# Kernel optimization log

Hardware: AMD Instinct MI355X
Metric: run time of the kernel (lower is better)

Reference implementation:

```python
import jax, jax.numpy as jnp
import numpy as np

NEG_SLOPE = 0.2


def setup_inputs() -> dict:
    key = jax.random.key(0)
    ks = jax.random.split(key, 12)
    N, D = 50000, 256
    H, C = 4, 128          # heads, per-head channels; H*C = gnn_hidden_dim = 512
    E = 800000
    edge_index = jax.random.randint(ks[0], (2, E), 0, N, dtype=jnp.int64)
    edge_weight = jax.random.uniform(ks[1], (E,), dtype=jnp.float32)
    s = 1.0 / np.sqrt(D)
    return {
        'edge_index': edge_index,
        'edge_weight': edge_weight,
        'emb':     jax.random.normal(ks[2], (N, D), jnp.float32),
        'W':       jax.random.normal(ks[3], (D, H * C), jnp.float32) * s,
        'att_src': jax.random.normal(ks[4], (H, C), jnp.float32) * s,
        'att_dst': jax.random.normal(ks[5], (H, C), jnp.float32) * s,
        'att_edge': jax.random.normal(ks[6], (H, C), jnp.float32) * s,
        'W_edge':  jax.random.normal(ks[7], (1, H * C), jnp.float32),
        'bias':    jnp.zeros((H * C,), jnp.float32),
        'W_out':   jax.random.normal(ks[8], (H * C, D), jnp.float32) * s,
        'b_out':   jnp.zeros((D,), jnp.float32),
    }


def reference(edge_index, edge_weight, emb, W, att_src, att_dst, att_edge,
              W_edge, bias, W_out, b_out):
    N, D = emb.shape
    H, C = att_src.shape
    src, dst = edge_index[0], edge_index[1]
    E = src.shape[0]

    # GATConv: shared linear projection for src and dst (in_channels is int)
    x = (emb @ W).reshape(N, H, C)                     # [N,H,C]

    # add self loops; edge_attr for loops = per-dst mean of incoming edge_attr
    ones = jnp.ones((E,), emb.dtype)
    cnt = jax.ops.segment_sum(ones, dst, num_segments=N)
    ea_mean = jax.ops.segment_sum(edge_weight, dst, num_segments=N) / jnp.maximum(cnt, 1.0)
    loop = jnp.arange(N, dtype=src.dtype)
    src_f = jnp.concatenate([src, loop])
    dst_f = jnp.concatenate([dst, loop])
    ea = jnp.concatenate([edge_weight, ea_mean])[:, None]   # [E+N, 1]

    e_feat = (ea @ W_edge).reshape(-1, H, C)            # [E+N,H,C]

    a_src = jnp.einsum('nhc,hc->nh', x, att_src)        # [N,H]
    a_dst = jnp.einsum('nhc,hc->nh', x, att_dst)
    a_e = jnp.einsum('ehc,hc->eh', e_feat, att_edge)    # [E+N,H]

    alpha = jax.nn.leaky_relu(a_src[src_f] + a_dst[dst_f] + a_e, NEG_SLOPE)
    # segment softmax over destination neighborhoods
    m = jax.ops.segment_max(alpha, dst_f, num_segments=N)
    alpha = jnp.exp(alpha - m[dst_f])
    denom = jax.ops.segment_sum(alpha, dst_f, num_segments=N)
    alpha = alpha / (denom[dst_f] + 1e-16)              # [E+N,H]

    msg = x[src_f] * alpha[..., None]                   # [E+N,H,C]
    out = jax.ops.segment_sum(msg, dst_f, num_segments=N).reshape(N, H * C) + bias

    return out @ W_out + b_out                          # [N,D]
```

## Files before the change

### kernel.cpp

```cpp
#include <hip/hip_runtime.h>
#include <cstdint>
#include <cstddef>

#define NEG_SLOPE 0.2f
#define HC 512
#define NH 4
#define CAP 64

typedef __attribute__((ext_vector_type(8))) short bf16x8;
typedef __attribute__((ext_vector_type(4))) float f32x4;

__device__ inline float lrelu(float z) { return z > 0.f ? z : NEG_SLOPE * z; }

__device__ inline unsigned short f2bf(float f) {
    unsigned u = __float_as_uint(f);
    u += 0x7FFFu + ((u >> 16) & 1u);
    return (unsigned short)(u >> 16);
}
__device__ inline float bflo(unsigned v) { return __uint_as_float(v << 16); }
__device__ inline float bfhi(unsigned v) { return __uint_as_float(v & 0xffff0000u); }

#define GLOAD16(gp, lp) \
    __builtin_amdgcn_global_load_lds( \
        (const __attribute__((address_space(1))) unsigned int*)(const void*)(gp), \
        (__attribute__((address_space(3))) unsigned int*)(void*)(lp), 16, 0, 0)

__global__ __launch_bounds__(256) void wprep_kernel(
        const float* __restrict__ W, const float* __restrict__ W_out,
        const float* __restrict__ att_s, const float* __restrict__ att_d,
        const float* __restrict__ W_edge, const float* __restrict__ att_edge,
        const float* __restrict__ bias, const float* __restrict__ b_out,
        const int* __restrict__ ei, const float* __restrict__ ew, int E,
        unsigned short* __restrict__ Wb, unsigned short* __restrict__ WoT,
        float* __restrict__ watt, float* __restrict__ bc4, float* __restrict__ sh,
        int* __restrict__ cnt, int2* __restrict__ csr2) {
    int b = blockIdx.x, t = threadIdx.x;
    if (b < 128) {
        int i = b * 256 + t;
        float4 v = reinterpret_cast<const float4*>(W)[i];
        ushort4 o;
        o.x = f2bf(v.x); o.y = f2bf(v.y); o.z = f2bf(v.z); o.w = f2bf(v.w);
        reinterpret_cast<ushort4*>(Wb)[i] = o;
    } else if (b < 640) {
        int idx = (b - 128) * 256 + t;
        int r = idx >> 8, c = idx & 255;
        WoT[(size_t)c * 512 + r] = f2bf(W_out[idx]);
    } else if (b < 648) {
        int i = b - 640;
        int h = i & 3;
        const float* att = (i < 4) ? att_s : att_d;
        float s = 0.f;
        for (int c = 0; c < 128; ++c)
            s += W[(size_t)t * HC + h * 128 + c] * att[h * 128 + c];
        watt[i * 256 + t] = s;
    } else if (b < 652) {
        int part = b - 648;
        int j0 = part * 128;
        float s = (part == 0) ? b_out[t] : 0.f;
        for (int j = j0; j < j0 + 128; ++j)
            s += bias[j] * W_out[(size_t)j * 256 + t];
        bc4[part * 256 + t] = s;
    } else if (b == 652) {
        if (t < NH) {
            float s = 0.f;
            for (int c = 0; c < 128; ++c)
                s += W_edge[t * 128 + c] * att_edge[t * 128 + c];
            sh[t] = s;
        }
    } else {
        int lane = t & 63;
        unsigned long long nzm = __ballot(ei[2 * lane + 1] != 0);
        int is64 = (nzm == 0ull) ? 1 : 0;
        int base = (b - 653) * 1024;

        int dv[4], sv[4];
        float wv[4];
        bool ok[4];
        #pragma unroll
        for (int r = 0; r < 4; ++r) {
            int e = base + r * 256 + t;
            ok[r] = (e < E);
            if (ok[r]) {
                size_t de = (size_t)E + e;
                dv[r] = is64 ? ei[2 * de] : ei[de];
                sv[r] = is64 ? ei[2 * (size_t)e] : ei[e];
                wv[r] = ew[e];
            }
        }
        int pos[4];
        #pragma unroll
        for (int r = 0; r < 4; ++r)
            if (ok[r]) pos[r] = atomicAdd(&cnt[dv[r]], 1);
        #pragma unroll
        for (int r = 0; r < 4; ++r)
            if (ok[r] && pos[r] < CAP)
                csr2[(size_t)dv[r] * CAP + pos[r]] =
                    make_int2(sv[r], __float_as_int(wv[r]));
    }
}

__global__ __launch_bounds__(256) void mt_kernel(
        const unsigned short* __restrict__ WoT, const unsigned short* __restrict__ Wb,
        unsigned short* __restrict__ MT) {
    __shared__ __align__(16) unsigned short As[128 * 64];
    __shared__ __align__(16) unsigned short Bs[128 * 64];
    int b = blockIdx.x, t = threadIdx.x;
    int lane = t & 63, w = t >> 6;
    int bn = (b & 1) * 128, bm = ((b >> 1) & 1) * 128, z = b >> 2;
    const unsigned short* A  = WoT + (size_t)z * 128;
    const unsigned short* BT = Wb  + (size_t)z * 128;
    int wr = w >> 1, wc = w & 1;

    f32x4 acc[4][4];
    #pragma unroll
    for (int i = 0; i < 4; ++i)
        #pragma unroll
        for (int j = 0; j < 4; ++j)
            acc[i][j] = (f32x4){0.f, 0.f, 0.f, 0.f};

    int lr = lane & 15, kb = lane >> 4;
    int q = lane & 7;

    for (int k0 = 0; k0 < 128; k0 += 64) {
        #pragma unroll
        for (int p = 0; p < 4; ++p) {
            int row = p * 32 + w * 8 + (lane >> 3);
            int ce  = ((q ^ (row & 7)) << 3) + k0;
            int ob  = p * 4096 + w * 1024;
            GLOAD16(A  + (size_t)(bm + row) * 512 + ce, (char*)As + ob);
            GLOAD16(BT + (size_t)(bn + row) * 512 + ce, (char*)Bs + ob);
        }
        __syncthreads();
        #pragma unroll
        for (int kk = 0; kk < 2; ++kk) {
            bf16x8 a[4], bfr[4];
            #pragma unroll
            for (int i = 0; i < 4; ++i) {
                int row = wr * 64 + i * 16 + lr;
                a[i] = *reinterpret_cast<const bf16x8*>(
                    &As[row * 64 + (((kk * 4 + kb) ^ (row & 7)) << 3)]);
            }
            #pragma unroll
            for (int j = 0; j < 4; ++j) {
                int row = wc * 64 + j * 16 + lr;
                bfr[j] = *reinterpret_cast<const bf16x8*>(
                    &Bs[row * 64 + (((kk * 4 + kb) ^ (row & 7)) << 3)]);
            }
            #pragma unroll
            for (int i = 0; i < 4; ++i)
                #pragma unroll
                for (int j = 0; j < 4; ++j)
                    acc[i][j] = __builtin_amdgcn_mfma_f32_16x16x32_bf16(a[i], bfr[j], acc[i][j], 0, 0, 0);
        }
        __syncthreads();
    }
    int rg = lane >> 4;
    #pragma unroll
    for (int i = 0; i < 4; ++i)
        #pragma unroll
        for (int r = 0; r < 4; ++r) {
            int row = bm + wr * 64 + i * 16 + rg * 4 + r;
            #pragma unroll
            for (int j = 0; j < 4; ++j) {
                int col = bn + wc * 64 + j * 16 + lr;
                MT[(size_t)row * 1024 + z * 256 + col] = f2bf(acc[i][j][r]);
            }
        }
}

__global__ __launch_bounds__(256) void embcast_kernel(
        const float4* __restrict__ embf4, const float* __restrict__ watt,
        uint2* __restrict__ embq, float* __restrict__ a_src,
        float* __restrict__ a_dst, int N) {
    int t = threadIdx.x;
    int wid = t >> 6, lane = t & 63;
    #pragma unroll
    for (int j = 0; j < 4; ++j) {
        int n = blockIdx.x * 16 + wid * 4 + j;
        if (n >= N) break;
        float4 v = embf4[(size_t)n * 64 + lane];
        uint2 o;
        o.x = (unsigned)f2bf(v.x) | ((unsigned)f2bf(v.y) << 16);
        o.y = (unsigned)f2bf(v.z) | ((unsigned)f2bf(v.w) << 16);
        embq[(size_t)n * 64 + lane] = o;
        float r[8];
        #pragma unroll
        for (int i = 0; i < 8; ++i) {
            float4 wv = reinterpret_cast<const float4*>(watt)[i * 64 + lane];
            r[i] = v.x * wv.x + v.y * wv.y + v.z * wv.z + v.w * wv.w;
        }
        #pragma unroll
        for (int off = 32; off > 0; off >>= 1) {
            #pragma unroll
            for (int i = 0; i < 8; ++i) r[i] += __shfl_xor(r[i], off);
        }
        if (lane == 0) {
            size_t bofs = (size_t)n * 4;
            a_src[bofs + 0] = r[0]; a_src[bofs + 1] = r[1];
            a_src[bofs + 2] = r[2]; a_src[bofs + 3] = r[3];
            a_dst[bofs + 0] = r[4]; a_dst[bofs + 1] = r[5];
            a_dst[bofs + 2] = r[6]; a_dst[bofs + 3] = r[7];
        }
    }
}

#define EFMA(W_, V_) { \
    float e0_ = bflo(V_.x), e1_ = bfhi(V_.x), e2_ = bflo(V_.y), e3_ = bfhi(V_.y); \
    a00 += W_.x * e0_; a01 += W_.x * e1_; a02 += W_.x * e2_; a03 += W_.x * e3_; \
    a10 += W_.y * e0_; a11 += W_.y * e1_; a12 += W_.y * e2_; a13 += W_.y * e3_; \
    a20 += W_.z * e0_; a21 += W_.z * e1_; a22 += W_.z * e2_; a23 += W_.z * e3_; \
    a30 += W_.w * e0_; a31 += W_.w * e1_; a32 += W_.w * e2_; a33 += W_.w * e3_; \
    den0 += W_.x; den1 += W_.y; den2 += W_.z; den3 += W_.w; }

__global__ __launch_bounds__(256) void agg_kernel(
        const uint2* __restrict__ embq, const float* __restrict__ a_src,
        const float* __restrict__ a_dst, const int* __restrict__ cnt,
        const float* __restrict__ sh, const int2* __restrict__ csr2,
        uint2* __restrict__ aggn, int N) {
    int wid = threadIdx.x >> 6, lane = threadIdx.x & 63;
    int n = blockIdx.x * 4 + wid;
    if (n >= N) return;
    int deg = cnt[n];
    int m = deg < CAP ? deg : CAP;

    __shared__ int s_src[4][64];
    __shared__ __align__(16) float s_alpha[4][64][4];

    int2 p;
    float wgt = 0.f;
    if (lane < m) {
        p = csr2[(size_t)n * CAP + lane];
        wgt = __int_as_float(p.y);
    }
    float wsl = wgt;
    #pragma unroll
    for (int o = 32; o > 0; o >>= 1) wsl += __shfl_xor(wsl, o);
    float eam = wsl / fmaxf((float)deg, 1.f);

    float ad0 = a_dst[(size_t)n * 4 + 0], ad1 = a_dst[(size_t)n * 4 + 1];
    float ad2 = a_dst[(size_t)n * 4 + 2], ad3 = a_dst[(size_t)n * 4 + 3];
    float sh0 = sh[0], sh1 = sh[1], sh2 = sh[2], sh3 = sh[3];
    float es0 = __expf(lrelu(a_src[(size_t)n * 4 + 0] + ad0 + eam * sh0));
    float es1 = __expf(lrelu(a_src[(size_t)n * 4 + 1] + ad1 + eam * sh1));
    float es2 = __expf(lrelu(a_src[(size_t)n * 4 + 2] + ad2 + eam * sh2));
    float es3 = __expf(lrelu(a_src[(size_t)n * 4 + 3] + ad3 + eam * sh3));

    uint2 xv = embq[(size_t)n * 64 + lane];
    float d0 = bflo(xv.x), d1 = bfhi(xv.x), d2 = bflo(xv.y), d3 = bfhi(xv.y);

    float a00 = es0 * d0, a01 = es0 * d1, a02 = es0 * d2, a03 = es0 * d3;
    float a10 = es1 * d0, a11 = es1 * d1, a12 = es1 * d2, a13 = es1 * d3;
    float a20 = es2 * d0, a21 = es2 * d1, a22 = es2 * d2, a23 = es2 * d3;
    float a30 = es3 * d0, a31 = es3 * d1, a32 = es3 * d2, a33 = es3 * d3;
    float den0 = es0, den1 = es1, den2 = es2, den3 = es3;

    if (lane < m) {
        int s = p.x;
        s_src[wid][lane] = s;
        float4 as4 = *reinterpret_cast<const float4*>(&a_src[(size_t)s * 4]);
        s_alpha[wid][lane][0] = __expf(lrelu(as4.x + ad0 + wgt * sh0));
        s_alpha[wid][lane][1] = __expf(lrelu(as4.y + ad1 + wgt * sh1));
        s_alpha[wid][lane][2] = __expf(lrelu(as4.z + ad2 + wgt * sh2));
        s_alpha[wid][lane][3] = __expf(lrelu(as4.w + ad3 + wgt * sh3));
    }
    int e2 = 0;
    for (; e2 + 2 <= m; e2 += 2) {
        int s0 = s_src[wid][e2], s1 = s_src[wid][e2 + 1];
        float4 w0 = *reinterpret_cast<const float4*>(s_alpha[wid][e2]);
        float4 w1 = *reinterpret_cast<const float4*>(s_alpha[wid][e2 + 1]);
        uint2 v0 = embq[(size_t)s0 * 64 + lane];
        uint2 v1 = embq[(size_t)s1 * 64 + lane];
        EFMA(w0, v0); EFMA(w1, v1);
    }
    if (e2 < m) {
        int s0 = s_src[wid][e2];
        float4 w0 = *reinterpret_cast<const float4*>(s_alpha[wid][e2]);
        uint2 v0 = embq[(size_t)s0 * 64 + lane];
        EFMA(w0, v0);
    }

    float i0 = 1.f / (den0 + 1e-16f), i1 = 1.f / (den1 + 1e-16f);
    float i2 = 1.f / (den2 + 1e-16f), i3 = 1.f / (den3 + 1e-16f);
    size_t base = (size_t)n * 256 + lane;
    uint2 o;
    o.x = (unsigned)f2bf(a00 * i0) | ((unsigned)f2bf(a01 * i0) << 16);
    o.y = (unsigned)f2bf(a02 * i0) | ((unsigned)f2bf(a03 * i0) << 16);
    aggn[base] = o;
    o.x = (unsigned)f2bf(a10 * i1) | ((unsigned)f2bf(a11 * i1) << 16);
    o.y = (unsigned)f2bf(a12 * i1) | ((unsigned)f2bf(a13 * i1) << 16);
    aggn[base + 64] = o;
    o.x = (unsigned)f2bf(a20 * i2) | ((unsigned)f2bf(a21 * i2) << 16);
    o.y = (unsigned)f2bf(a22 * i2) | ((unsigned)f2bf(a23 * i2) << 16);
    aggn[base + 128] = o;
    o.x = (unsigned)f2bf(a30 * i3) | ((unsigned)f2bf(a31 * i3) << 16);
    o.y = (unsigned)f2bf(a32 * i3) | ((unsigned)f2bf(a33 * i3) << 16);
    aggn[base + 192] = o;
}

__global__ __launch_bounds__(512) void gemm_out_kernel(
        const unsigned short* __restrict__ A,
        const unsigned short* __restrict__ BT,
        const float* __restrict__ bc4, float* __restrict__ C, int M) {
    __shared__ __align__(16) unsigned short As[128 * 64];
    __shared__ __align__(16) unsigned short Bs[256 * 64];
    int tid = threadIdx.x;
    int lane = tid & 63, w = tid >> 6;
    int bm = blockIdx.x * 128;
    int wr = w >> 2, wc = w & 3;

    f32x4 acc[4][4];
    #pragma unroll
    for (int i = 0; i < 4; ++i)
        #pragma unroll
        for (int j = 0; j < 4; ++j)
            acc[i][j] = (f32x4){0.f, 0.f, 0.f, 0.f};

    int lr = lane & 15, kb = lane >> 4;
    int q = lane & 7;

    for (int k0 = 0; k0 < 1024; k0 += 64) {
        #pragma unroll
        for (int p = 0; p < 2; ++p) {
            int row = p * 64 + w * 8 + (lane >> 3);
            int ce  = ((q ^ (row & 7)) << 3) + k0;
            int ob  = p * 8192 + w * 1024;
            int gr = bm + row; if (gr >= M) gr = M - 1;
            GLOAD16(A + (size_t)gr * 1024 + ce, (char*)As + ob);
        }
        #pragma unroll
        for (int p = 0; p < 4; ++p) {
            int row = p * 64 + w * 8 + (lane >> 3);
            int ce  = ((q ^ (row & 7)) << 3) + k0;
            int ob  = p * 8192 + w * 1024;
            GLOAD16(BT + (size_t)row * 1024 + ce, (char*)Bs + ob);
        }
        __syncthreads();

        #pragma unroll
        for (int kk = 0; kk < 2; ++kk) {
            bf16x8 a[4], b[4];
            #pragma unroll
            for (int i = 0; i < 4; ++i) {
                int row = wr * 64 + i * 16 + lr;
                a[i] = *reinterpret_cast<const bf16x8*>(
                    &As[row * 64 + (((kk * 4 + kb) ^ (row & 7)) << 3)]);
            }
            #pragma unroll
            for (int j = 0; j < 4; ++j) {
                int row = wc * 64 + j * 16 + lr;
                b[j] = *reinterpret_cast<const bf16x8*>(
                    &Bs[row * 64 + (((kk * 4 + kb) ^ (row & 7)) << 3)]);
            }
            #pragma unroll
            for (int i = 0; i < 4; ++i)
                #pragma unroll
                for (int j = 0; j < 4; ++j)
                    acc[i][j] = __builtin_amdgcn_mfma_f32_16x16x32_bf16(a[i], b[j], acc[i][j], 0, 0, 0);
        }
        __syncthreads();
    }

    int rg = lane >> 4;
    #pragma unroll
    for (int i = 0; i < 4; ++i) {
        #pragma unroll
        for (int r = 0; r < 4; ++r) {
            int row = bm + wr * 64 + i * 16 + rg * 4 + r;
            if (row >= M) continue;
            #pragma unroll
            for (int j = 0; j < 4; ++j) {
                int col = wc * 64 + j * 16 + lr;
                float bval = bc4[col] + bc4[256 + col] + bc4[512 + col] + bc4[768 + col];
                C[(size_t)row * 256 + col] = acc[i][j][r] + bval;
            }
        }
    }
}

extern "C" void kernel_launch(void* const* d_in, const int* in_sizes, int n_in,
                              void* d_out, int out_size, void* d_ws, size_t ws_size,
                              hipStream_t stream) {
    const int*   edge_index  = (const int*)d_in[0];
    const float* edge_weight = (const float*)d_in[1];
    const float* emb         = (const float*)d_in[2];
    const float* W           = (const float*)d_in[3];
    const float* att_src     = (const float*)d_in[4];
    const float* att_dst     = (const float*)d_in[5];
    const float* att_edge    = (const float*)d_in[6];
    const float* W_edge      = (const float*)d_in[7];
    const float* bias        = (const float*)d_in[8];
    const float* W_out       = (const float*)d_in[9];
    const float* b_out       = (const float*)d_in[10];
    float* out = (float*)d_out;

    const int E = in_sizes[1];
    const int D = 256;
    const int N = in_sizes[2] / D;
    const int mb = (N + 127) / 128;
    const int nEmb = (N + 15) / 16;
    const int nEdge4 = (E + 1023) / 1024;

    char* ws = (char*)d_ws;
    size_t off = 0;
    auto alloc = [&](size_t bytes) {
        size_t o = off;
        off += (bytes + 255) & ~(size_t)255;
        return o;
    };
    unsigned short* embb  = (unsigned short*)(ws + alloc((size_t)N * D * 2));
    unsigned short* aggn  = (unsigned short*)(ws + alloc((size_t)N * 1024 * 2));
    unsigned short* Wb    = (unsigned short*)(ws + alloc((size_t)D * HC * 2));
    unsigned short* WoT   = (unsigned short*)(ws + alloc((size_t)HC * D * 2));
    unsigned short* MT    = (unsigned short*)(ws + alloc((size_t)256 * 1024 * 2));
    float* watt    = (float*)(ws + alloc(2048 * 4));
    float* bc4     = (float*)(ws + alloc(1024 * 4));
    float* a_src   = (float*)(ws + alloc((size_t)N * 4 * 4));
    float* a_dst   = (float*)(ws + alloc((size_t)N * 4 * 4));
    float* sh      = (float*)(ws + alloc(64));
    size_t zbytes  = (size_t)N * 4;
    size_t zoff    = alloc(zbytes);
    int*   cnt     = (int*)(ws + zoff);
    int2*  csr2    = (int2*)(ws + alloc((size_t)N * CAP * 8));
    (void)ws_size; (void)n_in; (void)out_size;

    hipMemsetAsync(ws + zoff, 0, zbytes, stream);

    wprep_kernel<<<653 + nEdge4, 256, 0, stream>>>(
        W, W_out, att_src, att_dst, W_edge, att_edge, bias, b_out,
        edge_index, edge_weight, E, Wb, WoT, watt, bc4, sh, cnt, csr2);

    mt_kernel<<<16, 256, 0, stream>>>(WoT, Wb, MT);

    embcast_kernel<<<nEmb, 256, 0, stream>>>(
        (const float4*)emb, watt, (uint2*)embb, a_src, a_dst, N);

    agg_kernel<<<(N + 3) / 4, 256, 0, stream>>>(
        (const uint2*)embb, a_src, a_dst, cnt, sh, csr2, (uint2*)aggn, N);

    gemm_out_kernel<<<mb, 512, 0, stream>>>(aggn, MT, bc4, out, N);
}
```

Measured before the change: 226.5 us.

## Merge CSR build, weight-product GEMM and emb cast into one launch; fold memset into prep

The count-array memset moves into the weight-prep kernel as extra zeroing blocks. The edge CSR build, the small MT GEMM and the embedding bf16 cast/attention-dot kernel become one multi-role kernel dispatched by block index. This removes two launches and a memset and lets independent stages overlap on the GPU. The cost is that every block of the fused kernel reserves 32KB of shared memory, which may lower occupancy for the edge and cast blocks.

```diff
diff --git a/kernel.cpp b/kernel.cpp
--- a/kernel.cpp
+++ b/kernel.cpp
@@ -25,15 +25,14 @@
         (const __attribute__((address_space(1))) unsigned int*)(const void*)(gp), \
         (__attribute__((address_space(3))) unsigned int*)(void*)(lp), 16, 0, 0)
 
-__global__ __launch_bounds__(256) void wprep_kernel(
+__global__ __launch_bounds__(256) void prep0_kernel(
         const float* __restrict__ W, const float* __restrict__ W_out,
         const float* __restrict__ att_s, const float* __restrict__ att_d,
         const float* __restrict__ W_edge, const float* __restrict__ att_edge,
         const float* __restrict__ bias, const float* __restrict__ b_out,
-        const int* __restrict__ ei, const float* __restrict__ ew, int E,
         unsigned short* __restrict__ Wb, unsigned short* __restrict__ WoT,
         float* __restrict__ watt, float* __restrict__ bc4, float* __restrict__ sh,
-        int* __restrict__ cnt, int2* __restrict__ csr2) {
+        uint4* __restrict__ zptr, int zcount) {
     int b = blockIdx.x, t = threadIdx.x;
     if (b < 128) {
         int i = b * 256 + t;
@@ -68,10 +67,27 @@
             sh[t] = s;
         }
     } else {
+        int idx = (b - 653) * 256 + t;
+        if (idx < zcount) zptr[idx] = (uint4){0u, 0u, 0u, 0u};
+    }
+}
+
+__global__ __launch_bounds__(256) void mega_kernel(
+        const int* __restrict__ ei, const float* __restrict__ ew, int E,
+        int* __restrict__ cnt, int2* __restrict__ csr2,
+        const unsigned short* __restrict__ WoT, const unsigned short* __restrict__ Wb,
+        unsigned short* __restrict__ MT,
+        const float4* __restrict__ embf4, const float* __restrict__ watt,
+        uint2* __restrict__ embq, float* __restrict__ a_src,
+        float* __restrict__ a_dst, int N, int nEdge4) {
+    __shared__ __align__(16) char smem[32768];
+    int b = blockIdx.x, t = threadIdx.x;
+
+    if (b < nEdge4) {
         int lane = t & 63;
         unsigned long long nzm = __ballot(ei[2 * lane + 1] != 0);
         int is64 = (nzm == 0ull) ? 1 : 0;
-        int base = (b - 653) * 1024;
+        int base = b * 1024;
 
         int dv[4], sv[4];
         float wv[4];
@@ -96,110 +112,101 @@
             if (ok[r] && pos[r] < CAP)
                 csr2[(size_t)dv[r] * CAP + pos[r]] =
                     make_int2(sv[r], __float_as_int(wv[r]));
-    }
-}
-
-__global__ __launch_bounds__(256) void mt_kernel(
-        const unsigned short* __restrict__ WoT, const unsigned short* __restrict__ Wb,
-        unsigned short* __restrict__ MT) {
-    __shared__ __align__(16) unsigned short As[128 * 64];
-    __shared__ __align__(16) unsigned short Bs[128 * 64];
-    int b = blockIdx.x, t = threadIdx.x;
-    int lane = t & 63, w = t >> 6;
-    int bn = (b & 1) * 128, bm = ((b >> 1) & 1) * 128, z = b >> 2;
-    const unsigned short* A  = WoT + (size_t)z * 128;
-    const unsigned short* BT = Wb  + (size_t)z * 128;
-    int wr = w >> 1, wc = w & 1;
-
-    f32x4 acc[4][4];
-    #pragma unroll
-    for (int i = 0; i < 4; ++i)
-        #pragma unroll
-        for (int j = 0; j < 4; ++j)
-            acc[i][j] = (f32x4){0.f, 0.f, 0.f, 0.f};
-
-    int lr = lane & 15, kb = lane >> 4;
-    int q = lane & 7;
-
-    for (int k0 = 0; k0 < 128; k0 += 64) {
-        #pragma unroll
-        for (int p = 0; p < 4; ++p) {
-            int row = p * 32 + w * 8 + (lane >> 3);
-            int ce  = ((q ^ (row & 7)) << 3) + k0;
-            int ob  = p * 4096 + w * 1024;
-            GLOAD16(A  + (size_t)(bm + row) * 512 + ce, (char*)As + ob);
-            GLOAD16(BT + (size_t)(bn + row) * 512 + ce, (char*)Bs + ob);
-        }
-        __syncthreads();
-        #pragma unroll
-        for (int kk = 0; kk < 2; ++kk) {
-            bf16x8 a[4], bfr[4];
-            #pragma unroll
-            for (int i = 0; i < 4; ++i) {
-                int row = wr * 64 + i * 16 + lr;
-                a[i] = *reinterpret_cast<const bf16x8*>(
-                    &As[row * 64 + (((kk * 4 + kb) ^ (row & 7)) << 3)]);
-            }
-            #pragma unroll
-            for (int j = 0; j < 4; ++j) {
-                int row = wc * 64 + j * 16 + lr;
-                bfr[j] = *reinterpret_cast<const bf16x8*>(
-                    &Bs[row * 64 + (((kk * 4 + kb) ^ (row & 7)) << 3)]);
-            }
-            #pragma unroll
-            for (int i = 0; i < 4; ++i)
-                #pragma unroll
-                for (int j = 0; j < 4; ++j)
-                    acc[i][j] = __builtin_amdgcn_mfma_f32_16x16x32_bf16(a[i], bfr[j], acc[i][j], 0, 0, 0);
-        }
-        __syncthreads();
-    }
-    int rg = lane >> 4;
-    #pragma unroll
-    for (int i = 0; i < 4; ++i)
-        #pragma unroll
-        for (int r = 0; r < 4; ++r) {
-            int row = bm + wr * 64 + i * 16 + rg * 4 + r;
-            #pragma unroll
-            for (int j = 0; j < 4; ++j) {
-                int col = bn + wc * 64 + j * 16 + lr;
-                MT[(size_t)row * 1024 + z * 256 + col] = f2bf(acc[i][j][r]);
-            }
-        }
-}
-
-__global__ __launch_bounds__(256) void embcast_kernel(
-        const float4* __restrict__ embf4, const float* __restrict__ watt,
-        uint2* __restrict__ embq, float* __restrict__ a_src,
-        float* __restrict__ a_dst, int N) {
-    int t = threadIdx.x;
-    int wid = t >> 6, lane = t & 63;
-    #pragma unroll
-    for (int j = 0; j < 4; ++j) {
-        int n = blockIdx.x * 16 + wid * 4 + j;
-        if (n >= N) break;
-        float4 v = embf4[(size_t)n * 64 + lane];
-        uint2 o;
-        o.x = (unsigned)f2bf(v.x) | ((unsigned)f2bf(v.y) << 16);
-        o.y = (unsigned)f2bf(v.z) | ((unsigned)f2bf(v.w) << 16);
-        embq[(size_t)n * 64 + lane] = o;
-        float r[8];
-        #pragma unroll
-        for (int i = 0; i < 8; ++i) {
-            float4 wv = reinterpret_cast<const float4*>(watt)[i * 64 + lane];
-            r[i] = v.x * wv.x + v.y * wv.y + v.z * wv.z + v.w * wv.w;
-        }
-        #pragma unroll
-        for (int off = 32; off > 0; off >>= 1) {
-            #pragma unroll
-            for (int i = 0; i < 8; ++i) r[i] += __shfl_xor(r[i], off);
-        }
-        if (lane == 0) {
-            size_t bofs = (size_t)n * 4;
-            a_src[bofs + 0] = r[0]; a_src[bofs + 1] = r[1];
-            a_src[bofs + 2] = r[2]; a_src[bofs + 3] = r[3];
-            a_dst[bofs + 0] = r[4]; a_dst[bofs + 1] = r[5];
-            a_dst[bofs + 2] = r[6]; a_dst[bofs + 3] = r[7];
+    } else if (b < nEdge4 + 16) {
+        int bb = b - nEdge4;
+        unsigned short* As = (unsigned short*)smem;
+        unsigned short* Bs = (unsigned short*)(smem + 16384);
+        int lane = t & 63, w = t >> 6;
+        int bn = (bb & 1) * 128, bm = ((bb >> 1) & 1) * 128, z = bb >> 2;
+        const unsigned short* A  = WoT + (size_t)z * 128;
+        const unsigned short* BT = Wb  + (size_t)z * 128;
+        int wr = w >> 1, wc = w & 1;
+
+        f32x4 acc[4][4];
+        #pragma unroll
+        for (int i = 0; i < 4; ++i)
+            #pragma unroll
+            for (int j = 0; j < 4; ++j)
+                acc[i][j] = (f32x4){0.f, 0.f, 0.f, 0.f};
+
+        int lr = lane & 15, kb = lane >> 4;
+        int q = lane & 7;
+
+        for (int k0 = 0; k0 < 128; k0 += 64) {
+            #pragma unroll
+            for (int p = 0; p < 4; ++p) {
+                int row = p * 32 + w * 8 + (lane >> 3);
+                int ce  = ((q ^ (row & 7)) << 3) + k0;
+                int ob  = p * 4096 + w * 1024;
+                GLOAD16(A  + (size_t)(bm + row) * 512 + ce, (char*)As + ob);
+                GLOAD16(BT + (size_t)(bn + row) * 512 + ce, (char*)Bs + ob);
+            }
+            __syncthreads();
+            #pragma unroll
+            for (int kk = 0; kk < 2; ++kk) {
+                bf16x8 a[4], bfr[4];
+                #pragma unroll
+                for (int i = 0; i < 4; ++i) {
+                    int row = wr * 64 + i * 16 + lr;
+                    a[i] = *reinterpret_cast<const bf16x8*>(
+                        &As[row * 64 + (((kk * 4 + kb) ^ (row & 7)) << 3)]);
+                }
+                #pragma unroll
+                for (int j = 0; j < 4; ++j) {
+                    int row = wc * 64 + j * 16 + lr;
+                    bfr[j] = *reinterpret_cast<const bf16x8*>(
+                        &Bs[row * 64 + (((kk * 4 + kb) ^ (row & 7)) << 3)]);
+                }
+                #pragma unroll
+                for (int i = 0; i < 4; ++i)
+                    #pragma unroll
+                    for (int j = 0; j < 4; ++j)
+                        acc[i][j] = __builtin_amdgcn_mfma_f32_16x16x32_bf16(a[i], bfr[j], acc[i][j], 0, 0, 0);
+            }
+            __syncthreads();
+        }
+        int rg = lane >> 4;
+        #pragma unroll
+        for (int i = 0; i < 4; ++i)
+            #pragma unroll
+            for (int r = 0; r < 4; ++r) {
+                int row = bm + wr * 64 + i * 16 + rg * 4 + r;
+                #pragma unroll
+                for (int j = 0; j < 4; ++j) {
+                    int col = bn + wc * 64 + j * 16 + lr;
+                    MT[(size_t)row * 1024 + z * 256 + col] = f2bf(acc[i][j][r]);
+                }
+            }
+    } else {
+        int bb = b - nEdge4 - 16;
+        int wid = t >> 6, lane = t & 63;
+        #pragma unroll
+        for (int j = 0; j < 4; ++j) {
+            int n = bb * 16 + wid * 4 + j;
+            if (n >= N) break;
+            float4 v = embf4[(size_t)n * 64 + lane];
+            uint2 o;
+            o.x = (unsigned)f2bf(v.x) | ((unsigned)f2bf(v.y) << 16);
+            o.y = (unsigned)f2bf(v.z) | ((unsigned)f2bf(v.w) << 16);
+            embq[(size_t)n * 64 + lane] = o;
+            float r[8];
+            #pragma unroll
+            for (int i = 0; i < 8; ++i) {
+                float4 wv = reinterpret_cast<const float4*>(watt)[i * 64 + lane];
+                r[i] = v.x * wv.x + v.y * wv.y + v.z * wv.z + v.w * wv.w;
+            }
+            #pragma unroll
+            for (int off = 32; off > 0; off >>= 1) {
+                #pragma unroll
+                for (int i = 0; i < 8; ++i) r[i] += __shfl_xor(r[i], off);
+            }
+            if (lane == 0) {
+                size_t bofs = (size_t)n * 4;
+                a_src[bofs + 0] = r[0]; a_src[bofs + 1] = r[1];
+                a_src[bofs + 2] = r[2]; a_src[bofs + 3] = r[3];
+                a_dst[bofs + 0] = r[4]; a_dst[bofs + 1] = r[5];
+                a_dst[bofs + 2] = r[6]; a_dst[bofs + 3] = r[7];
+            }
         }
     }
 }
@@ -417,22 +424,22 @@
     float* a_src   = (float*)(ws + alloc((size_t)N * 4 * 4));
     float* a_dst   = (float*)(ws + alloc((size_t)N * 4 * 4));
     float* sh      = (float*)(ws + alloc(64));
-    size_t zbytes  = (size_t)N * 4;
+    size_t zbytes  = ((size_t)N * 4 + 15) & ~(size_t)15;
     size_t zoff    = alloc(zbytes);
     int*   cnt     = (int*)(ws + zoff);
     int2*  csr2    = (int2*)(ws + alloc((size_t)N * CAP * 8));
     (void)ws_size; (void)n_in; (void)out_size;
 
-    hipMemsetAsync(ws + zoff, 0, zbytes, stream);
-
-    wprep_kernel<<<653 + nEdge4, 256, 0, stream>>>(
+    int zcount = (int)(zbytes / 16);
+    int nz = (zcount + 255) / 256;
+
+    prep0_kernel<<<653 + nz, 256, 0, stream>>>(
         W, W_out, att_src, att_dst, W_edge, att_edge, bias, b_out,
-        edge_index, edge_weight, E, Wb, WoT, watt, bc4, sh, cnt, csr2);
-
-    mt_kernel<<<16, 256, 0, stream>>>(WoT, Wb, MT);
-
-    embcast_kernel<<<nEmb, 256, 0, stream>>>(
-        (const float4*)emb, watt, (uint2*)embb, a_src, a_dst, N);
+        Wb, WoT, watt, bc4, sh, (uint4*)(ws + zoff), zcount);
+
+    mega_kernel<<<nEdge4 + 16 + nEmb, 256, 0, stream>>>(
+        edge_index, edge_weight, E, cnt, csr2, WoT, Wb, MT,
+        (const float4*)emb, watt, (uint2*)embb, a_src, a_dst, N, nEdge4);
 
     agg_kernel<<<(N + 3) / 4, 256, 0, stream>>>(
         (const uint2*)embb, a_src, a_dst, cnt, sh, csr2, (uint2*)aggn, N);
```

Result: no change. 223.8 us (-1.2%).

## Merge prep kernels into two interleaved launches and sort edges per destination

Applied to the files above, without the earlier changes.

Folds weight prep, edge CSR build and the embedding bf16 cast into one launch, with edge blocks interleaved among aux blocks by index modulo six. The small MT GEMM and the attention-score pass share a second launch. This cuts launch count and lets independent work overlap. Attention scores are now computed from the bf16-cast embeddings rather than fp32, which slightly changes precision. The aggregation kernel adds a 64-lane bitonic sort of each node's incoming edges by source index, which gives a deterministic summation order and possibly better gather locality, at the cost of extra shuffles per node.

```diff
diff --git a/kernel.cpp b/kernel.cpp
--- a/kernel.cpp
+++ b/kernel.cpp
@@ -25,53 +25,25 @@
         (const __attribute__((address_space(1))) unsigned int*)(const void*)(gp), \
         (__attribute__((address_space(3))) unsigned int*)(void*)(lp), 16, 0, 0)
 
-__global__ __launch_bounds__(256) void wprep_kernel(
+__global__ __launch_bounds__(256) void mega1_kernel(
+        const int* __restrict__ ei, const float* __restrict__ ew, int E,
+        int* __restrict__ cnt, int2* __restrict__ csr2,
         const float* __restrict__ W, const float* __restrict__ W_out,
         const float* __restrict__ att_s, const float* __restrict__ att_d,
         const float* __restrict__ W_edge, const float* __restrict__ att_edge,
         const float* __restrict__ bias, const float* __restrict__ b_out,
-        const int* __restrict__ ei, const float* __restrict__ ew, int E,
         unsigned short* __restrict__ Wb, unsigned short* __restrict__ WoT,
         float* __restrict__ watt, float* __restrict__ bc4, float* __restrict__ sh,
-        int* __restrict__ cnt, int2* __restrict__ csr2) {
+        const float4* __restrict__ embf4, uint2* __restrict__ embq,
+        int nQuads, int nCast) {
     int b = blockIdx.x, t = threadIdx.x;
-    if (b < 128) {
-        int i = b * 256 + t;
-        float4 v = reinterpret_cast<const float4*>(W)[i];
-        ushort4 o;
-        o.x = f2bf(v.x); o.y = f2bf(v.y); o.z = f2bf(v.z); o.w = f2bf(v.w);
-        reinterpret_cast<ushort4*>(Wb)[i] = o;
-    } else if (b < 640) {
-        int idx = (b - 128) * 256 + t;
-        int r = idx >> 8, c = idx & 255;
-        WoT[(size_t)c * 512 + r] = f2bf(W_out[idx]);
-    } else if (b < 648) {
-        int i = b - 640;
-        int h = i & 3;
-        const float* att = (i < 4) ? att_s : att_d;
-        float s = 0.f;
-        for (int c = 0; c < 128; ++c)
-            s += W[(size_t)t * HC + h * 128 + c] * att[h * 128 + c];
-        watt[i * 256 + t] = s;
-    } else if (b < 652) {
-        int part = b - 648;
-        int j0 = part * 128;
-        float s = (part == 0) ? b_out[t] : 0.f;
-        for (int j = j0; j < j0 + 128; ++j)
-            s += bias[j] * W_out[(size_t)j * 256 + t];
-        bc4[part * 256 + t] = s;
-    } else if (b == 652) {
-        if (t < NH) {
-            float s = 0.f;
-            for (int c = 0; c < 128; ++c)
-                s += W_edge[t * 128 + c] * att_edge[t * 128 + c];
-            sh[t] = s;
-        }
-    } else {
+    int r6 = b % 6, q6 = b / 6;
+
+    if (r6 == 0) {
         int lane = t & 63;
         unsigned long long nzm = __ballot(ei[2 * lane + 1] != 0);
         int is64 = (nzm == 0ull) ? 1 : 0;
-        int base = (b - 653) * 1024;
+        int base = q6 * 1024;
 
         int dv[4], sv[4];
         float wv[4];
@@ -96,110 +68,157 @@
             if (ok[r] && pos[r] < CAP)
                 csr2[(size_t)dv[r] * CAP + pos[r]] =
                     make_int2(sv[r], __float_as_int(wv[r]));
-    }
-}
-
-__global__ __launch_bounds__(256) void mt_kernel(
+        return;
+    }
+
+    int aux = q6 * 5 + r6 - 1;
+    if (aux < 128) {
+        int i = aux * 256 + t;
+        float4 v = reinterpret_cast<const float4*>(W)[i];
+        ushort4 o;
+        o.x = f2bf(v.x); o.y = f2bf(v.y); o.z = f2bf(v.z); o.w = f2bf(v.w);
+        reinterpret_cast<ushort4*>(Wb)[i] = o;
+    } else if (aux < 640) {
+        int idx = (aux - 128) * 256 + t;
+        int r = idx >> 8, c = idx & 255;
+        WoT[(size_t)c * 512 + r] = f2bf(W_out[idx]);
+    } else if (aux < 648) {
+        int i = aux - 640;
+        int h = i & 3;
+        const float* att = (i < 4) ? att_s : att_d;
+        float s = 0.f;
+        for (int c = 0; c < 128; ++c)
+            s += W[(size_t)t * HC + h * 128 + c] * att[h * 128 + c];
+        watt[i * 256 + t] = s;
+    } else if (aux < 652) {
+        int part = aux - 648;
+        int j0 = part * 128;
+        float s = (part == 0) ? b_out[t] : 0.f;
+        for (int j = j0; j < j0 + 128; ++j)
+            s += bias[j] * W_out[(size_t)j * 256 + t];
+        bc4[part * 256 + t] = s;
+    } else if (aux == 652) {
+        if (t < NH) {
+            float s = 0.f;
+            for (int c = 0; c < 128; ++c)
+                s += W_edge[t * 128 + c] * att_edge[t * 128 + c];
+            sh[t] = s;
+        }
+    } else if (aux < 653 + nCast) {
+        int base = (aux - 653) * 1024;
+        #pragma unroll
+        for (int j = 0; j < 4; ++j) {
+            int i = base + j * 256 + t;
+            if (i < nQuads) {
+                float4 v = embf4[i];
+                uint2 o;
+                o.x = (unsigned)f2bf(v.x) | ((unsigned)f2bf(v.y) << 16);
+                o.y = (unsigned)f2bf(v.z) | ((unsigned)f2bf(v.w) << 16);
+                embq[i] = o;
+            }
+        }
+    }
+}
+
+__global__ __launch_bounds__(256) void mega2_kernel(
         const unsigned short* __restrict__ WoT, const unsigned short* __restrict__ Wb,
-        unsigned short* __restrict__ MT) {
-    __shared__ __align__(16) unsigned short As[128 * 64];
-    __shared__ __align__(16) unsigned short Bs[128 * 64];
+        unsigned short* __restrict__ MT,
+        const uint2* __restrict__ embq, const float* __restrict__ watt,
+        float* __restrict__ a_src, float* __restrict__ a_dst, int N) {
+    __shared__ __align__(16) char smem[32768];
     int b = blockIdx.x, t = threadIdx.x;
-    int lane = t & 63, w = t >> 6;
-    int bn = (b & 1) * 128, bm = ((b >> 1) & 1) * 128, z = b >> 2;
-    const unsigned short* A  = WoT + (size_t)z * 128;
-    const unsigned short* BT = Wb  + (size_t)z * 128;
-    int wr = w >> 1, wc = w & 1;
-
-    f32x4 acc[4][4];
-    #pragma unroll
-    for (int i = 0; i < 4; ++i)
-        #pragma unroll
-        for (int j = 0; j < 4; ++j)
-            acc[i][j] = (f32x4){0.f, 0.f, 0.f, 0.f};
-
-    int lr = lane & 15, kb = lane >> 4;
-    int q = lane & 7;
-
-    for (int k0 = 0; k0 < 128; k0 += 64) {
-        #pragma unroll
-        for (int p = 0; p < 4; ++p) {
-            int row = p * 32 + w * 8 + (lane >> 3);
-            int ce  = ((q ^ (row & 7)) << 3) + k0;
-            int ob  = p * 4096 + w * 1024;
-            GLOAD16(A  + (size_t)(bm + row) * 512 + ce, (char*)As + ob);
-            GLOAD16(BT + (size_t)(bn + row) * 512 + ce, (char*)Bs + ob);
-        }
-        __syncthreads();
-        #pragma unroll
-        for (int kk = 0; kk < 2; ++kk) {
-            bf16x8 a[4], bfr[4];
-            #pragma unroll
-            for (int i = 0; i < 4; ++i) {
-                int row = wr * 64 + i * 16 + lr;
-                a[i] = *reinterpret_cast<const bf16x8*>(
-                    &As[row * 64 + (((kk * 4 + kb) ^ (row & 7)) << 3)]);
-            }
-            #pragma unroll
-            for (int j = 0; j < 4; ++j) {
-                int row = wc * 64 + j * 16 + lr;
-                bfr[j] = *reinterpret_cast<const bf16x8*>(
-                    &Bs[row * 64 + (((kk * 4 + kb) ^ (row & 7)) << 3)]);
-            }
-            #pragma unroll
-            for (int i = 0; i < 4; ++i)
-                #pragma unroll
-                for (int j = 0; j < 4; ++j)
-                    acc[i][j] = __builtin_amdgcn_mfma_f32_16x16x32_bf16(a[i], bfr[j], acc[i][j], 0, 0, 0);
-        }
-        __syncthreads();
-    }
-    int rg = lane >> 4;
-    #pragma unroll
-    for (int i = 0; i < 4; ++i)
-        #pragma unroll
-        for (int r = 0; r < 4; ++r) {
-            int row = bm + wr * 64 + i * 16 + rg * 4 + r;
-            #pragma unroll
-            for (int j = 0; j < 4; ++j) {
-                int col = bn + wc * 64 + j * 16 + lr;
-                MT[(size_t)row * 1024 + z * 256 + col] = f2bf(acc[i][j][r]);
-            }
-        }
-}
-
-__global__ __launch_bounds__(256) void embcast_kernel(
-        const float4* __restrict__ embf4, const float* __restrict__ watt,
-        uint2* __restrict__ embq, float* __restrict__ a_src,
-        float* __restrict__ a_dst, int N) {
-    int t = threadIdx.x;
-    int wid = t >> 6, lane = t & 63;
-    #pragma unroll
-    for (int j = 0; j < 4; ++j) {
-        int n = blockIdx.x * 16 + wid * 4 + j;
-        if (n >= N) break;
-        float4 v = embf4[(size_t)n * 64 + lane];
-        uint2 o;
-        o.x = (unsigned)f2bf(v.x) | ((unsigned)f2bf(v.y) << 16);
-        o.y = (unsigned)f2bf(v.z) | ((unsigned)f2bf(v.w) << 16);
-        embq[(size_t)n * 64 + lane] = o;
-        float r[8];
-        #pragma unroll
-        for (int i = 0; i < 8; ++i) {
-            float4 wv = reinterpret_cast<const float4*>(watt)[i * 64 + lane];
-            r[i] = v.x * wv.x + v.y * wv.y + v.z * wv.z + v.w * wv.w;
-        }
-        #pragma unroll
-        for (int off = 32; off > 0; off >>= 1) {
-            #pragma unroll
-            for (int i = 0; i < 8; ++i) r[i] += __shfl_xor(r[i], off);
-        }
-        if (lane == 0) {
-            size_t bofs = (size_t)n * 4;
-            a_src[bofs + 0] = r[0]; a_src[bofs + 1] = r[1];
-            a_src[bofs + 2] = r[2]; a_src[bofs + 3] = r[3];
-            a_dst[bofs + 0] = r[4]; a_dst[bofs + 1] = r[5];
-            a_dst[bofs + 2] = r[6]; a_dst[bofs + 3] = r[7];
+
+    if (b < 16) {
+        unsigned short* As = (unsigned short*)smem;
+        unsigned short* Bs = (unsigned short*)(smem + 16384);
+        int lane = t & 63, w = t >> 6;
+        int bn = (b & 1) * 128, bm = ((b >> 1) & 1) * 128, z = b >> 2;
+        const unsigned short* A  = WoT + (size_t)z * 128;
+        const unsigned short* BT = Wb  + (size_t)z * 128;
+        int wr = w >> 1, wc = w & 1;
+
+        f32x4 acc[4][4];
+        #pragma unroll
+        for (int i = 0; i < 4; ++i)
+            #pragma unroll
+            for (int j = 0; j < 4; ++j)
+                acc[i][j] = (f32x4){0.f, 0.f, 0.f, 0.f};
+
+        int lr = lane & 15, kb = lane >> 4;
+        int q = lane & 7;
+
+        for (int k0 = 0; k0 < 128; k0 += 64) {
+            #pragma unroll
+            for (int p = 0; p < 4; ++p) {
+                int row = p * 32 + w * 8 + (lane >> 3);
+                int ce  = ((q ^ (row & 7)) << 3) + k0;
+                int ob  = p * 4096 + w * 1024;
+                GLOAD16(A  + (size_t)(bm + row) * 512 + ce, (char*)As + ob);
+                GLOAD16(BT + (size_t)(bn + row) * 512 + ce, (char*)Bs + ob);
+            }
+            __syncthreads();
+            #pragma unroll
+            for (int kk = 0; kk < 2; ++kk) {
+                bf16x8 a[4], bfr[4];
+                #pragma unroll
+                for (int i = 0; i < 4; ++i) {
+                    int row = wr * 64 + i * 16 + lr;
+                    a[i] = *reinterpret_cast<const bf16x8*>(
+                        &As[row * 64 + (((kk * 4 + kb) ^ (row & 7)) << 3)]);
+                }
+                #pragma unroll
+                for (int j = 0; j < 4; ++j) {
+                    int row = wc * 64 + j * 16 + lr;
+                    bfr[j] = *reinterpret_cast<const bf16x8*>(
+                        &Bs[row * 64 + (((kk * 4 + kb) ^ (row & 7)) << 3)]);
+                }
+                #pragma unroll
+                for (int i = 0; i < 4; ++i)
+                    #pragma unroll
+                    for (int j = 0; j < 4; ++j)
+                        acc[i][j] = __builtin_amdgcn_mfma_f32_16x16x32_bf16(a[i], bfr[j], acc[i][j], 0, 0, 0);
+            }
+            __syncthreads();
+        }
+        int rg = lane >> 4;
+        #pragma unroll
+        for (int i = 0; i < 4; ++i)
+            #pragma unroll
+            for (int r = 0; r < 4; ++r) {
+                int row = bm + wr * 64 + i * 16 + rg * 4 + r;
+                #pragma unroll
+                for (int j = 0; j < 4; ++j) {
+                    int col = bn + wc * 64 + j * 16 + lr;
+                    MT[(size_t)row * 1024 + z * 256 + col] = f2bf(acc[i][j][r]);
+                }
+            }
+    } else {
+        int bb = b - 16;
+        int wid = t >> 6, lane = t & 63;
+        #pragma unroll
+        for (int j = 0; j < 4; ++j) {
+            int n = bb * 16 + wid * 4 + j;
+            if (n >= N) break;
+            uint2 v = embq[(size_t)n * 64 + lane];
+            float d0 = bflo(v.x), d1 = bfhi(v.x), d2 = bflo(v.y), d3 = bfhi(v.y);
+            float r[8];
+            #pragma unroll
+            for (int i = 0; i < 8; ++i) {
+                float4 wv = reinterpret_cast<const float4*>(watt)[i * 64 + lane];
+                r[i] = d0 * wv.x + d1 * wv.y + d2 * wv.z + d3 * wv.w;
+            }
+            #pragma unroll
+            for (int off = 32; off > 0; off >>= 1) {
+                #pragma unroll
+                for (int i = 0; i < 8; ++i) r[i] += __shfl_xor(r[i], off);
+            }
+            if (lane == 0) {
+                size_t bofs = (size_t)n * 4;
+                a_src[bofs + 0] = r[0]; a_src[bofs + 1] = r[1];
+                a_src[bofs + 2] = r[2]; a_src[bofs + 3] = r[3];
+                a_dst[bofs + 0] = r[4]; a_dst[bofs + 1] = r[5];
+                a_dst[bofs + 2] = r[6]; a_dst[bofs + 3] = r[7];
+            }
         }
     }
 }
@@ -226,12 +245,25 @@
     __shared__ int s_src[4][64];
     __shared__ __align__(16) float s_alpha[4][64][4];
 
-    int2 p;
-    float wgt = 0.f;
+    int k1 = 0x7FFFFFFF, k2 = 0x7FFFFFFF;
     if (lane < m) {
-        p = csr2[(size_t)n * CAP + lane];
-        wgt = __int_as_float(p.y);
-    }
+        int2 p = csr2[(size_t)n * CAP + lane];
+        k1 = p.x; k2 = p.y;
+    }
+    #pragma unroll
+    for (int k = 2; k <= 64; k <<= 1) {
+        #pragma unroll
+        for (int j = k >> 1; j > 0; j >>= 1) {
+            int o1 = __shfl_xor(k1, j);
+            int o2 = __shfl_xor(k2, j);
+            bool lower = (lane & j) == 0;
+            bool asc = (lane & k) == 0;
+            bool cmp = (k1 > o1) || (k1 == o1 && k2 > o2);
+            if ((cmp == lower) == asc) { k1 = o1; k2 = o2; }
+        }
+    }
+    float wgt = (lane < m) ? __int_as_float(k2) : 0.f;
+
     float wsl = wgt;
     #pragma unroll
     for (int o = 32; o > 0; o >>= 1) wsl += __shfl_xor(wsl, o);
@@ -255,7 +287,7 @@
     float den0 = es0, den1 = es1, den2 = es2, den3 = es3;
 
     if (lane < m) {
-        int s = p.x;
+        int s = k1;
         s_src[wid][lane] = s;
         float4 as4 = *reinterpret_cast<const float4*>(&a_src[(size_t)s * 4]);
         s_alpha[wid][lane][0] = __expf(lrelu(as4.x + ad0 + wgt * sh0));
@@ -399,6 +431,8 @@
     const int mb = (N + 127) / 128;
     const int nEmb = (N + 15) / 16;
     const int nEdge4 = (E + 1023) / 1024;
+    const int nQuads = N * 64;
+    const int nCast = (nQuads + 1023) / 1024;
 
     char* ws = (char*)d_ws;
     size_t off = 0;
@@ -425,14 +459,14 @@
 
     hipMemsetAsync(ws + zoff, 0, zbytes, stream);
 
-    wprep_kernel<<<653 + nEdge4, 256, 0, stream>>>(
+    mega1_kernel<<<nEdge4 * 6, 256, 0, stream>>>(
+        edge_index, edge_weight, E, cnt, csr2,
         W, W_out, att_src, att_dst, W_edge, att_edge, bias, b_out,
-        edge_index, edge_weight, E, Wb, WoT, watt, bc4, sh, cnt, csr2);
-
-    mt_kernel<<<16, 256, 0, stream>>>(WoT, Wb, MT);
-
-    embcast_kernel<<<nEmb, 256, 0, stream>>>(
-        (const float4*)emb, watt, (uint2*)embb, a_src, a_dst, N);
+        Wb, WoT, watt, bc4, sh,
+        (const float4*)emb, (uint2*)embb, nQuads, nCast);
+
+    mega2_kernel<<<16 + nEmb, 256, 0, stream>>>(
+        WoT, Wb, MT, (const uint2*)embb, watt, a_src, a_dst, N);
 
     agg_kernel<<<(N + 3) / 4, 256, 0, stream>>>(
         (const uint2*)embb, a_src, a_dst, cnt, sh, csr2, (uint2*)aggn, N);
```

After: 231.3 us. 2.1% more time.
